# Performance work log

Measured on AMD Instinct MI355X. Metric: run time of the kernel, lower is better.

## Reference

```python
import jax, jax.numpy as jnp
import numpy as np

H = 2304; I_FF = 9216; NH = 8; NKV = 4; HD = 256; W = 4096; V = 65536
EPS = 1e-6; SOFTCAP = 30.0; HALF = HD // 2; POS = W // 2  # current decode position
WSCALE = 0.02


def rmsnorm(x, w, eps=EPS):
    return x * jax.lax.rsqrt(jnp.mean(x * x, axis=-1, keepdims=True) + eps) * w


def setup_inputs() -> dict:
    key = jax.random.key(0)
    ks = jax.random.split(key, 16)
    # RoPE angles for position POS
    inv_freq = 1.0 / (10000.0 ** (jnp.arange(HALF, dtype=jnp.float32) / HALF))
    ang = POS * inv_freq
    # attention mask: allow slots <= POS, block the rest
    slot = jnp.arange(W)
    mask = jnp.where(slot <= POS, 0.0, -1e9).astype(jnp.float32).reshape(1, 1, 1, W)
    # one-hot scatter selector for the cache write
    update_idx = jnp.zeros((1, 1, W, 1), jnp.float32).at[0, 0, POS, 0].set(1.0)
    return {
        "hidden_prev": jax.random.normal(ks[0], (1, 1, H), jnp.float32),
        "embed_token": jax.random.normal(ks[1], (1, 1, H), jnp.float32),
        "kv_k_in": jax.random.normal(ks[2], (1, NKV, W, HD), jnp.float32),
        "kv_v_in": jax.random.normal(ks[3], (1, NKV, W, HD), jnp.float32),
        "cos": jnp.cos(ang),
        "sin": jnp.sin(ang),
        "mask": mask,
        "update_idx": update_idx,
        "in_h_w": jax.random.normal(ks[4], (H, H), jnp.float32) * WSCALE,
        "in_e_w": jax.random.normal(ks[5], (H, H), jnp.float32) * WSCALE,
        "input_ln_w": jnp.ones((H,), jnp.float32),
        "post_attn_ln_w": jnp.ones((H,), jnp.float32),
        "pre_ffn_ln_w": jnp.ones((H,), jnp.float32),
        "post_ffn_ln_w": jnp.ones((H,), jnp.float32),
        "final_ln_w": jnp.ones((H,), jnp.float32),
        "q_w": jax.random.normal(ks[6], (NH * HD, H), jnp.float32) * WSCALE,
        "k_w": jax.random.normal(ks[7], (NKV * HD, H), jnp.float32) * WSCALE,
        "v_w": jax.random.normal(ks[8], (NKV * HD, H), jnp.float32) * WSCALE,
        "o_w": jax.random.normal(ks[9], (H, NH * HD), jnp.float32) * WSCALE,
        "q_norm_w": jnp.ones((HD,), jnp.float32),
        "k_norm_w": jnp.ones((HD,), jnp.float32),
        "gate_w": jax.random.normal(ks[10], (I_FF, H), jnp.float32) * WSCALE,
        "up_w": jax.random.normal(ks[11], (I_FF, H), jnp.float32) * WSCALE,
        "down_w": jax.random.normal(ks[12], (H, I_FF), jnp.float32) * WSCALE,
        "lm_head_w": jax.random.normal(ks[13], (V, H), jnp.float32) * WSCALE,
    }


def reference(hidden_prev, embed_token, kv_k_in, kv_v_in, cos, sin, mask, update_idx,
              in_h_w, in_e_w, input_ln_w, post_attn_ln_w, pre_ffn_ln_w, post_ffn_ln_w,
              final_ln_w, q_w, k_w, v_w, o_w, q_norm_w, k_norm_w, gate_w, up_w, down_w,
              lm_head_w):
    # dual input projection (1x1 convs == linear)
    x = hidden_prev @ in_h_w.T + embed_token @ in_e_w.T          # [1,1,H]
    residual = x
    hn = rmsnorm(x, input_ln_w)
    # QKV
    q = (hn @ q_w.T).reshape(1, NH, 1, HD)
    k = (hn @ k_w.T).reshape(1, NKV, 1, HD)
    v = (hn @ v_w.T).reshape(1, NKV, 1, HD)
    q = rmsnorm(q, q_norm_w)
    k = rmsnorm(k, k_norm_w)
    # RoPE (half-split rotation)
    cos_r = cos.reshape(1, 1, 1, HALF)
    sin_r = sin.reshape(1, 1, 1, HALF)
    q1, q2 = q[..., :HALF], q[..., HALF:]
    q = jnp.concatenate([q1 * cos_r - q2 * sin_r, q2 * cos_r + q1 * sin_r], axis=-1)
    k1, k2 = k[..., :HALF], k[..., HALF:]
    k_rot = jnp.concatenate([k1 * cos_r - k2 * sin_r, k2 * cos_r + k1 * sin_r], axis=-1)
    # multiply-based KV cache update
    keep = 1.0 - update_idx                                      # [1,1,W,1]
    kv_k_out = kv_k_in * keep + k_rot * update_idx               # [1,NKV,W,HD]
    kv_v_out = kv_v_in * keep + v * update_idx
    # GQA expansion
    n_rep = NH // NKV
    k_exp = jnp.repeat(kv_k_out, n_rep, axis=1)                  # [1,NH,W,HD]
    v_exp = jnp.repeat(kv_v_out, n_rep, axis=1)
    # fp32 attention
    scale = 1.0 / np.sqrt(HD)
    attn = jnp.einsum('bhqd,bhkd->bhqk', q, k_exp) * scale + mask
    p = jax.nn.softmax(attn, axis=-1)
    out = jnp.einsum('bhqk,bhkd->bhqd', p, v_exp).reshape(1, 1, NH * HD)
    h_attn = rmsnorm(out @ o_w.T, post_attn_ln_w)
    x = residual + h_attn
    residual = x
    # FFN (gelu-gated)
    hf = rmsnorm(x, pre_ffn_ln_w)
    d = (jax.nn.gelu(hf @ gate_w.T, approximate=False) * (hf @ up_w.T)) @ down_w.T
    x = residual + rmsnorm(d, post_ffn_ln_w)
    hidden_out = rmsnorm(x, final_ln_w)
    # lm_head + softcap + argmax
    logits = hidden_out @ lm_head_w.T                            # [1,1,V]
    logits = jnp.tanh(logits / SOFTCAP) * SOFTCAP
    idx = jnp.argmax(logits, axis=-1)                            # [1,1]
    top_k_indices = idx.reshape(1).astype(jnp.int32)
    top_k_values = jnp.take_along_axis(logits, idx[..., None], axis=-1).reshape(1)
    return (top_k_indices, top_k_values, hidden_out, kv_k_out, kv_v_out)
```

## Files before the change

### kernel.cpp

```cpp
#include <hip/hip_runtime.h>
#include <math.h>

#define H      2304
#define I_FF   9216
#define NH     8
#define NKV    4
#define HD     256
#define W_CTX  4096
#define V_SZ   65536
#define POS    2048
#define NCHUNK 32
#define CHUNK  64
#define NATTN  (NH * NCHUNK)
#define NBLK_ATTN_TOTAL 2048
#define EPS    1e-6f
#define NBLK_IN   576
#define NBLK_LM   4096

enum {
  WS_X    = 0,
  WS_SSQ  = 2304,
  WS_QKV  = 2880,
  WS_ML   = 6976,
  WS_YP   = 7488,
  WS_HRAW = 73024,
  WS_X2   = 75328,
  WS_ACT  = 77632,
  WS_DV   = 86848,
  WS_PART = 89152,
  WS_END  = 97344
};

typedef float f4v __attribute__((ext_vector_type(4)));
typedef float f2v __attribute__((ext_vector_type(2)));

__device__ __forceinline__ f4v ntload4(const float* p) {
  return __builtin_nontemporal_load((const f4v*)p);
}
__device__ __forceinline__ float wave_reduce_sum(float v) {
#pragma unroll
  for (int off = 32; off; off >>= 1) v += __shfl_down(v, off);
  return v;
}
__device__ __forceinline__ float wave_reduce_max(float v) {
#pragma unroll
  for (int off = 32; off; off >>= 1) v = fmaxf(v, __shfl_down(v, off));
  return v;
}
__device__ __forceinline__ float dot4(float4 a, float4 b) {
  return a.x * b.x + a.y * b.y + a.z * b.z + a.w * b.w;
}
__device__ __forceinline__ float dot4n(f4v a, float4 b) {
  return a.x * b.x + a.y * b.y + a.z * b.z + a.w * b.w;
}

__global__ void k_input(const float* __restrict__ Wh, const float* __restrict__ We,
                        const float* __restrict__ hprev, const float* __restrict__ emb,
                        float* __restrict__ x, float* __restrict__ ssq_part) {
  __shared__ float sv[4];
  int wv = threadIdx.x >> 6, lane = threadIdx.x & 63;
  int row = blockIdx.x * 4 + wv;
  const float* wh = Wh + (size_t)row * H;
  const float* we = We + (size_t)row * H;
  const float4* hp = (const float4*)hprev;
  const float4* em = (const float4*)emb;
  float acc = 0.f;
#pragma unroll
  for (int i = 0; i < H / 256; ++i) {
    int idx = lane + i * 64;
    acc += dot4n(ntload4(wh + idx * 4), hp[idx]);
    acc += dot4n(ntload4(we + idx * 4), em[idx]);
  }
  acc = wave_reduce_sum(acc);
  if (lane == 0) { x[row] = acc; sv[wv] = acc * acc; }
  __syncthreads();
  if (threadIdx.x == 0) ssq_part[blockIdx.x] = sv[0] + sv[1] + sv[2] + sv[3];
}

__global__ void k_qkv(const float* __restrict__ qw, const float* __restrict__ kw,
                      const float* __restrict__ vw, const float* __restrict__ x,
                      const float* __restrict__ lnw, const float* __restrict__ ssq,
                      float* __restrict__ qkv) {
  __shared__ float sred[4];
  int tid = threadIdx.x, lane = tid & 63, wv = tid >> 6;
  int row = (blockIdx.x * 256 + tid) >> 6;
  const float* Wrow;
  if (row < 2048)      Wrow = qw + (size_t)row * H;
  else if (row < 3072) Wrow = kw + (size_t)(row - 2048) * H;
  else                 Wrow = vw + (size_t)(row - 3072) * H;
  f4v p0 = ntload4(Wrow + lane * 4);
  float s = ssq[tid] + ssq[tid + 256] + (tid < 64 ? ssq[tid + 512] : 0.f);
  s = wave_reduce_sum(s);
  if (lane == 0) sred[wv] = s;
  __syncthreads();
  float scale = rsqrtf((sred[0] + sred[1] + sred[2] + sred[3]) / (float)H + EPS);

  const float4* xv = (const float4*)x;
  const float4* l4 = (const float4*)lnw;
  float4 hx0 = xv[lane], wl0 = l4[lane];
  float acc = p0.x * (hx0.x * scale * wl0.x) + p0.y * (hx0.y * scale * wl0.y) +
              p0.z * (hx0.z * scale * wl0.z) + p0.w * (hx0.w * scale * wl0.w);
#pragma unroll
  for (int i = 1; i < H / 256; ++i) {
    int idx = lane + i * 64;
    f4v w = ntload4(Wrow + idx * 4);
    float4 hx = xv[idx], wl = l4[idx];
    acc += w.x * (hx.x * scale * wl.x) + w.y * (hx.y * scale * wl.y) +
           w.z * (hx.z * scale * wl.z) + w.w * (hx.w * scale * wl.w);
  }
  acc = wave_reduce_sum(acc);
  if (lane == 0) qkv[row] = acc;
}

__global__ void k_attn(const float* __restrict__ qkv, const float* __restrict__ qnw,
                       const float* __restrict__ knw, const float* __restrict__ cosv,
                       const float* __restrict__ sinv, const float* __restrict__ kin,
                       const float* __restrict__ vin, float* __restrict__ kv_k_out,
                       float* __restrict__ kv_v_out, float* __restrict__ ml,
                       float* __restrict__ ypart,
                       const f2v* __restrict__ kin2, const f2v* __restrict__ vin2,
                       f2v* __restrict__ kout2, f2v* __restrict__ vout2) {
  int b = blockIdx.x;
  int tid = threadIdx.x, lane = tid & 63, wv = tid >> 6;
  if (b >= NATTN) {
    size_t cb = b - NATTN;
    const size_t n = (size_t)NKV * W_CTX * HD / 2;
    const size_t stride = (size_t)(NBLK_ATTN_TOTAL - NATTN) * 256;
    for (size_t i = cb * 256 + tid; i < n; i += stride) {
      int slot = (int)((i >> 7) & (W_CTX - 1));
      if (slot != POS) {
        __builtin_nontemporal_store(kin2[i], kout2 + i);
        __builtin_nontemporal_store(vin2[i], vout2 + i);
      }
    }
    return;
  }
  int h = b >> 5, j = b & 31, kvh = h >> 1;
  __shared__ float qs[HD], ks[HD], sc[CHUNK + 1];
  __shared__ float sredq[4], sredk[4];
  float qv = qkv[h * HD + tid];
  float kv = qkv[2048 + kvh * HD + tid];
  float pq = wave_reduce_sum(qv * qv);
  float pk = wave_reduce_sum(kv * kv);
  if (lane == 0) { sredq[wv] = pq; sredk[wv] = pk; }
  __syncthreads();
  float sq = rsqrtf((sredq[0] + sredq[1] + sredq[2] + sredq[3]) / (float)HD + EPS);
  float sk = rsqrtf((sredk[0] + sredk[1] + sredk[2] + sredk[3]) / (float)HD + EPS);
  qs[tid] = qv * sq * qnw[tid];
  ks[tid] = kv * sk * knw[tid];
  __syncthreads();
  if (tid < HD / 2) {
    float c = cosv[tid], s2 = sinv[tid];
    float q1 = qs[tid], q2 = qs[tid + 128];
    qs[tid] = q1 * c - q2 * s2;  qs[tid + 128] = q2 * c + q1 * s2;
    float k1 = ks[tid], k2 = ks[tid + 128];
    ks[tid] = k1 * c - k2 * s2;  ks[tid + 128] = k2 * c + k1 * s2;
  }
  __syncthreads();
  if (j == 0 && (h & 1) == 0) {
    kv_k_out[((size_t)kvh * W_CTX + POS) * HD + tid] = ks[tid];
    kv_v_out[((size_t)kvh * W_CTX + POS) * HD + tid] = qkv[3072 + kvh * HD + tid];
  }
  int base = j * CHUNK;
  int clen = (j == NCHUNK - 1) ? CHUNK + 1 : CHUNK;
  float4 qf = ((const float4*)qs)[lane];
  const float4* Kb = (const float4*)(kin + ((size_t)kvh * W_CTX + base) * HD);
  for (int i = wv; i < clen; i += 4) {
    float4 kk = (i < CHUNK) ? Kb[(size_t)i * (HD / 4) + lane] : ((const float4*)ks)[lane];
    float acc = dot4(qf, kk);
    acc = wave_reduce_sum(acc);
    if (lane == 0) sc[i] = acc * 0.0625f;
  }
  __syncthreads();
  float m = -1e30f;
  for (int i = tid; i < clen; i += 256) m = fmaxf(m, sc[i]);
  m = wave_reduce_max(m);
  if (lane == 0) sredq[wv] = m;
  __syncthreads();
  float M = fmaxf(fmaxf(sredq[0], sredq[1]), fmaxf(sredq[2], sredq[3]));
  float ssum = 0.f;
  for (int i = tid; i < clen; i += 256) { float e = expf(sc[i] - M); sc[i] = e; ssum += e; }
  ssum = wave_reduce_sum(ssum);
  if (lane == 0) sredk[wv] = ssum;
  __syncthreads();
  if (tid == 0) {
    ml[(h * NCHUNK + j) * 2]     = M;
    ml[(h * NCHUNK + j) * 2 + 1] = sredk[0] + sredk[1] + sredk[2] + sredk[3];
  }
  const float* Vb = vin + ((size_t)kvh * W_CTX + base) * HD;
  float a0 = 0.f, a1 = 0.f, a2 = 0.f, a3 = 0.f;
  for (int s = 0; s < CHUNK; s += 4) {
    a0 += sc[s]     * Vb[(size_t)s * HD + tid];
    a1 += sc[s + 1] * Vb[(size_t)(s + 1) * HD + tid];
    a2 += sc[s + 2] * Vb[(size_t)(s + 2) * HD + tid];
    a3 += sc[s + 3] * Vb[(size_t)(s + 3) * HD + tid];
  }
  if (clen > CHUNK) a0 += sc[CHUNK] * qkv[3072 + kvh * HD + tid];
  ypart[(size_t)(h * NCHUNK + j) * HD + tid] = a0 + a1 + a2 + a3;
}

__global__ void k_o(const float* __restrict__ ow, const float* __restrict__ ml,
                    const float* __restrict__ yp, float* __restrict__ hraw) {
  __shared__ float lmm[256], lml[256], ew[256], Lh[8];
  __shared__ float atts[NH * HD];
  int tid = threadIdx.x, lane = tid & 63, wv = tid >> 6;
  lmm[tid] = ml[2 * tid];
  lml[tid] = ml[2 * tid + 1];
  __syncthreads();
  int hh = tid >> 5;
  float M = -1e30f;
#pragma unroll 8
  for (int jj = 0; jj < 32; ++jj) M = fmaxf(M, lmm[hh * 32 + jj]);
  ew[tid] = expf(lmm[tid] - M);
  __syncthreads();
  if ((tid & 31) == 0) {
    float L = 0.f;
#pragma unroll 8
    for (int jj = 0; jj < 32; ++jj) L += lml[tid + jj] * ew[tid + jj];
    Lh[tid >> 5] = L;
  }
  __syncthreads();
#pragma unroll
  for (int ho = 0; ho < 2; ++ho) {
    int h2 = 2 * wv + ho;
    float4 acc = make_float4(0.f, 0.f, 0.f, 0.f);
#pragma unroll 8
    for (int jj = 0; jj < 32; ++jj) {
      const float4* yr = (const float4*)(yp + (size_t)(h2 * 32 + jj) * HD);
      float4 v = yr[lane];
      float w = ew[h2 * 32 + jj];
      acc.x += w * v.x; acc.y += w * v.y; acc.z += w * v.z; acc.w += w * v.w;
    }
    float invL = 1.f / Lh[h2];
    float4 r = make_float4(acc.x * invL, acc.y * invL, acc.z * invL, acc.w * invL);
    ((float4*)atts)[h2 * (HD / 4) + lane] = r;
  }
  __syncthreads();
  int row = blockIdx.x * 4 + wv;
  const float* wr = ow + (size_t)row * (NH * HD);
  const float4* xv = (const float4*)atts;
  float acc = 0.f;
#pragma unroll
  for (int i = 0; i < (NH * HD) / 256; ++i) {
    int idx = lane + i * 64;
    acc += dot4n(ntload4(wr + idx * 4), xv[idx]);
  }
  acc = wave_reduce_sum(acc);
  if (lane == 0) hraw[row] = acc;
}

__global__ void k_gateup(const float* __restrict__ gw, const float* __restrict__ uw,
                         const float* __restrict__ x, const float* __restrict__ hraw,
                         const float* __restrict__ w_post, const float* __restrict__ w_pre,
                         float* __restrict__ x2_out, float* __restrict__ act) {
  __shared__ float hfs[H];
  __shared__ float srA[4], srB[4];
  int tid = threadIdx.x, lane = tid & 63, wv = tid >> 6;
  int r0 = (blockIdx.x * 4 + wv) * 2;
  const float* g0 = gw + (size_t)r0 * H;
  const float* g1 = gw + (size_t)(r0 + 1) * H;
  const float* u0 = uw + (size_t)r0 * H;
  const float* u1 = uw + (size_t)(r0 + 1) * H;
  f4v pg0 = ntload4(g0 + lane * 4), pg1 = ntload4(g1 + lane * 4);
  f4v pu0 = ntload4(u0 + lane * 4), pu1 = ntload4(u1 + lane * 4);
  float lh[9], lx2[9];
  float ss = 0.f;
#pragma unroll
  for (int k = 0; k < 9; ++k) { lh[k] = hraw[tid + k * 256]; ss += lh[k] * lh[k]; }
  ss = wave_reduce_sum(ss);
  if (lane == 0) srA[wv] = ss;
  __syncthreads();
  float sc1 = rsqrtf((srA[0] + srA[1] + srA[2] + srA[3]) / (float)H + EPS);
  float ss2 = 0.f;
#pragma unroll
  for (int k = 0; k < 9; ++k) {
    int i = tid + k * 256;
    float v = x[i] + lh[k] * sc1 * w_post[i];
    lx2[k] = v; ss2 += v * v;
  }
  ss2 = wave_reduce_sum(ss2);
  if (lane == 0) srB[wv] = ss2;
  __syncthreads();
  float sc2 = rsqrtf((srB[0] + srB[1] + srB[2] + srB[3]) / (float)H + EPS);
#pragma unroll
  for (int k = 0; k < 9; ++k) { int i = tid + k * 256; hfs[i] = lx2[k] * sc2 * w_pre[i]; }
  if (blockIdx.x == 0) {
#pragma unroll
    for (int k = 0; k < 9; ++k) { int i = tid + k * 256; x2_out[i] = lx2[k]; }
  }
  __syncthreads();
  const float4* h4 = (const float4*)hfs;
  float4 hh0 = h4[lane];
  float ag0 = dot4n(pg0, hh0), ag1 = dot4n(pg1, hh0);
  float au0 = dot4n(pu0, hh0), au1 = dot4n(pu1, hh0);
#pragma unroll
  for (int i = 1; i < H / 256; ++i) {
    int idx = lane + i * 64;
    float4 hh = h4[idx];
    ag0 += dot4n(ntload4(g0 + idx * 4), hh);
    ag1 += dot4n(ntload4(g1 + idx * 4), hh);
    au0 += dot4n(ntload4(u0 + idx * 4), hh);
    au1 += dot4n(ntload4(u1 + idx * 4), hh);
  }
  ag0 = wave_reduce_sum(ag0);
  ag1 = wave_reduce_sum(ag1);
  au0 = wave_reduce_sum(au0);
  au1 = wave_reduce_sum(au1);
  if (lane == 0) {
    float gl0 = 0.5f * ag0 * (1.f + erff(ag0 * 0.70710678118f));
    float gl1 = 0.5f * ag1 * (1.f + erff(ag1 * 0.70710678118f));
    act[r0]     = gl0 * au0;
    act[r0 + 1] = gl1 * au1;
  }
}

__global__ void k_down(const float* __restrict__ dw, const float* __restrict__ actv,
                       float* __restrict__ dv) {
  int row  = (blockIdx.x * 256 + threadIdx.x) >> 6;
  int lane = threadIdx.x & 63;
  const float* wr = dw + (size_t)row * I_FF;
  const float4* xv = (const float4*)actv;
  float acc = 0.f;
#pragma unroll 4
  for (int i = 0; i < I_FF / 256; ++i) {
    int idx = lane + i * 64;
    acc += dot4n(ntload4(wr + idx * 4), xv[idx]);
  }
  acc = wave_reduce_sum(acc);
  if (lane == 0) dv[row] = acc;
}

__global__ void k_lmhead(const float* __restrict__ Wm, const float* __restrict__ x2,
                         const float* __restrict__ dv, const float* __restrict__ w_post,
                         const float* __restrict__ w_fin, float* __restrict__ hid_out,
                         float2* __restrict__ partials) {
  __shared__ float hid[H];
  __shared__ float srA[4], srB[4];
  __shared__ float bv[4]; __shared__ int bi[4];
  int tid = threadIdx.x, lane = tid & 63, wv = tid >> 6;
  int gw   = (blockIdx.x * 256 + tid) >> 6;
  int row0 = gw * 4;
  const float* w0 = Wm + (size_t)(row0 + 0) * H;
  const float* w1 = Wm + (size_t)(row0 + 1) * H;
  const float* w2 = Wm + (size_t)(row0 + 2) * H;
  const float* w3 = Wm + (size_t)(row0 + 3) * H;
  f4v p0 = ntload4(w0 + lane * 4), p1 = ntload4(w1 + lane * 4);
  f4v p2 = ntload4(w2 + lane * 4), p3 = ntload4(w3 + lane * 4);
  float ld[9], lx3[9];
  float ss = 0.f;
#pragma unroll
  for (int k = 0; k < 9; ++k) { ld[k] = dv[tid + k * 256]; ss += ld[k] * ld[k]; }
  ss = wave_reduce_sum(ss);
  if (lane == 0) srA[wv] = ss;
  __syncthreads();
  float sc1 = rsqrtf((srA[0] + srA[1] + srA[2] + srA[3]) / (float)H + EPS);
  float ss2 = 0.f;
#pragma unroll
  for (int k = 0; k < 9; ++k) {
    int i = tid + k * 256;
    float v = x2[i] + ld[k] * sc1 * w_post[i];
    lx3[k] = v; ss2 += v * v;
  }
  ss2 = wave_reduce_sum(ss2);
  if (lane == 0) srB[wv] = ss2;
  __syncthreads();
  float sc2 = rsqrtf((srB[0] + srB[1] + srB[2] + srB[3]) / (float)H + EPS);
#pragma unroll
  for (int k = 0; k < 9; ++k) { int i = tid + k * 256; hid[i] = lx3[k] * sc2 * w_fin[i]; }
  if (blockIdx.x == 0) {
#pragma unroll
    for (int k = 0; k < 9; ++k) { int i = tid + k * 256; hid_out[i] = hid[i]; }
  }
  __syncthreads();
  const float4* hv = (const float4*)hid;
  float4 b0 = hv[lane];
  float a0 = dot4n(p0, b0), a1 = dot4n(p1, b0);
  float a2 = dot4n(p2, b0), a3 = dot4n(p3, b0);
#pragma unroll
  for (int i = 1; i < H / 256; ++i) {
    int idx = lane + i * 64;
    float4 b = hv[idx];
    a0 += dot4n(ntload4(w0 + idx * 4), b);
    a1 += dot4n(ntload4(w1 + idx * 4), b);
    a2 += dot4n(ntload4(w2 + idx * 4), b);
    a3 += dot4n(ntload4(w3 + idx * 4), b);
  }
  a0 = wave_reduce_sum(a0);
  a1 = wave_reduce_sum(a1);
  a2 = wave_reduce_sum(a2);
  a3 = wave_reduce_sum(a3);
  if (lane == 0) {
    float l0 = 30.f * tanhf(a0 * (1.f / 30.f));
    float l1 = 30.f * tanhf(a1 * (1.f / 30.f));
    float l2 = 30.f * tanhf(a2 * (1.f / 30.f));
    float l3 = 30.f * tanhf(a3 * (1.f / 30.f));
    float best = l0; int bidx = row0;
    if (l1 > best) { best = l1; bidx = row0 + 1; }
    if (l2 > best) { best = l2; bidx = row0 + 2; }
    if (l3 > best) { best = l3; bidx = row0 + 3; }
    bv[wv] = best; bi[wv] = bidx;
  }
  __syncthreads();
  if (tid == 0) {
    float B = bv[0]; int I = bi[0];
    for (int i = 1; i < 4; ++i)
      if (bv[i] > B || (bv[i] == B && bi[i] < I)) { B = bv[i]; I = bi[i]; }
    partials[blockIdx.x] = make_float2(B, (float)I);
  }
}

__global__ void k_argmax_final(const float2* __restrict__ partials, int n,
                               float* __restrict__ out) {
  __shared__ float bv[256]; __shared__ int bi[256];
  int tid = threadIdx.x;
  float best = -1e30f; int bidx = 0x7fffffff;
  for (int i = tid; i < n; i += 256) {
    float2 p = partials[i];
    int pi = (int)p.y;
    if (p.x > best || (p.x == best && pi < bidx)) { best = p.x; bidx = pi; }
  }
  bv[tid] = best; bi[tid] = bidx; __syncthreads();
  for (int s = 128; s; s >>= 1) {
    if (tid < s) {
      if (bv[tid + s] > bv[tid] || (bv[tid + s] == bv[tid] && bi[tid + s] < bi[tid])) {
        bv[tid] = bv[tid + s]; bi[tid] = bi[tid + s];
      }
    }
    __syncthreads();
  }
  if (tid == 0) { out[0] = (float)bi[0]; out[1] = bv[0]; }
}

extern "C" void kernel_launch(void* const* d_in, const int* in_sizes, int n_in,
                              void* d_out, int out_size, void* d_ws, size_t ws_size,
                              hipStream_t stream) {
  const float* hidden_prev = (const float*)d_in[0];
  const float* embed_token = (const float*)d_in[1];
  const float* kv_k_in     = (const float*)d_in[2];
  const float* kv_v_in     = (const float*)d_in[3];
  const float* cosv        = (const float*)d_in[4];
  const float* sinv        = (const float*)d_in[5];
  const float* in_h_w      = (const float*)d_in[8];
  const float* in_e_w      = (const float*)d_in[9];
  const float* input_ln_w  = (const float*)d_in[10];
  const float* post_attn_w = (const float*)d_in[11];
  const float* pre_ffn_w   = (const float*)d_in[12];
  const float* post_ffn_w  = (const float*)d_in[13];
  const float* final_ln_w  = (const float*)d_in[14];
  const float* q_w         = (const float*)d_in[15];
  const float* k_w         = (const float*)d_in[16];
  const float* v_w         = (const float*)d_in[17];
  const float* o_w         = (const float*)d_in[18];
  const float* q_norm_w    = (const float*)d_in[19];
  const float* k_norm_w    = (const float*)d_in[20];
  const float* gate_w      = (const float*)d_in[21];
  const float* up_w        = (const float*)d_in[22];
  const float* down_w      = (const float*)d_in[23];
  const float* lm_head_w   = (const float*)d_in[24];

  float* out     = (float*)d_out;
  float* out_hid = out + 2;
  float* out_kvk = out + 2 + H;
  float* out_kvv = out_kvk + (size_t)NKV * W_CTX * HD;
  float* ws      = (float*)d_ws;

  k_input<<<NBLK_IN, 256, 0, stream>>>(in_h_w, in_e_w, hidden_prev, embed_token,
                                       ws + WS_X, ws + WS_SSQ);
  k_qkv<<<1024, 256, 0, stream>>>(q_w, k_w, v_w, ws + WS_X, input_ln_w,
                                  ws + WS_SSQ, ws + WS_QKV);
  k_attn<<<NBLK_ATTN_TOTAL, 256, 0, stream>>>(
      ws + WS_QKV, q_norm_w, k_norm_w, cosv, sinv, kv_k_in, kv_v_in,
      out_kvk, out_kvv, ws + WS_ML, ws + WS_YP,
      (const f2v*)kv_k_in, (const f2v*)kv_v_in, (f2v*)out_kvk, (f2v*)out_kvv);
  k_o<<<H / 4, 256, 0, stream>>>(o_w, ws + WS_ML, ws + WS_YP, ws + WS_HRAW);
  k_gateup<<<I_FF / 8, 256, 0, stream>>>(gate_w, up_w, ws + WS_X, ws + WS_HRAW,
                                         post_attn_w, pre_ffn_w, ws + WS_X2, ws + WS_ACT);
  k_down<<<H / 4, 256, 0, stream>>>(down_w, ws + WS_ACT, ws + WS_DV);
  k_lmhead<<<NBLK_LM, 256, 0, stream>>>(lm_head_w, ws + WS_X2, ws + WS_DV,
                                        post_ffn_w, final_ln_w, out_hid,
                                        (float2*)(ws + WS_PART));
  k_argmax_final<<<1, 256, 0, stream>>>((const float2*)(ws + WS_PART), NBLK_LM, out);

  (void)in_sizes; (void)n_in; (void)out_size; (void)ws_size;
}
```

Measured before the change: 196.2 us.

## Widen lm_head rows per wave, fold argmax into atomicMax, halve attention chunks

The lm_head kernel now has each wave compute 8 vocab rows instead of 4, which halves the block count. It drops the separate partials array and argmax kernel by packing an order-preserving float key with the inverted index into a 64-bit atomicMax, and tanh is applied only once to the winning raw logit. Attention uses 16 chunks of 128 slots instead of 32 of 64, and the combine in k_o is adjusted to match. This reduces reduction traffic and per-block overhead, at the cost of more registers per wave and fewer attention blocks, which means less parallelism per head.

```diff
diff --git a/kernel.cpp b/kernel.cpp
--- a/kernel.cpp
+++ b/kernel.cpp
@@ -9,26 +9,26 @@
 #define W_CTX  4096
 #define V_SZ   65536
 #define POS    2048
-#define NCHUNK 32
-#define CHUNK  64
+#define NCHUNK 16
+#define CHUNK  128
 #define NATTN  (NH * NCHUNK)
 #define NBLK_ATTN_TOTAL 2048
 #define EPS    1e-6f
 #define NBLK_IN   576
-#define NBLK_LM   4096
+#define NBLK_LM   2048
 
 enum {
   WS_X    = 0,
   WS_SSQ  = 2304,
-  WS_QKV  = 2880,
-  WS_ML   = 6976,
-  WS_YP   = 7488,
-  WS_HRAW = 73024,
-  WS_X2   = 75328,
-  WS_ACT  = 77632,
-  WS_DV   = 86848,
-  WS_PART = 89152,
-  WS_END  = 97344
+  WS_AMAX = 2880,
+  WS_QKV  = 2896,
+  WS_ML   = 6992,
+  WS_YP   = 7248,
+  WS_HRAW = 40016,
+  WS_X2   = 42320,
+  WS_ACT  = 44624,
+  WS_DV   = 53840,
+  WS_END  = 56144
 };
 
 typedef float f4v __attribute__((ext_vector_type(4)));
@@ -53,10 +53,16 @@
 __device__ __forceinline__ float dot4n(f4v a, float4 b) {
   return a.x * b.x + a.y * b.y + a.z * b.z + a.w * b.w;
 }
+__device__ __forceinline__ unsigned int fkey(float v) {
+  unsigned int b = __float_as_uint(v);
+  return (b & 0x80000000u) ? ~b : (b | 0x80000000u);
+}
 
 __global__ void k_input(const float* __restrict__ Wh, const float* __restrict__ We,
                         const float* __restrict__ hprev, const float* __restrict__ emb,
-                        float* __restrict__ x, float* __restrict__ ssq_part) {
+                        float* __restrict__ x, float* __restrict__ ssq_part,
+                        unsigned long long* __restrict__ amax) {
+  if (blockIdx.x == 0 && threadIdx.x == 0) amax[0] = 0ull;
   __shared__ float sv[4];
   int wv = threadIdx.x >> 6, lane = threadIdx.x & 63;
   int row = blockIdx.x * 4 + wv;
@@ -135,7 +141,7 @@
     }
     return;
   }
-  int h = b >> 5, j = b & 31, kvh = h >> 1;
+  int h = b >> 4, j = b & 15, kvh = h >> 1;
   __shared__ float qs[HD], ks[HD], sc[CHUNK + 1];
   __shared__ float sredq[4], sredk[4];
   float qv = qkv[h * HD + tid];
@@ -201,39 +207,40 @@
 
 __global__ void k_o(const float* __restrict__ ow, const float* __restrict__ ml,
                     const float* __restrict__ yp, float* __restrict__ hraw) {
-  __shared__ float lmm[256], lml[256], ew[256], Lh[8];
+  __shared__ float lmm[128], lml[128], ew[128], Lh[8];
   __shared__ float atts[NH * HD];
   int tid = threadIdx.x, lane = tid & 63, wv = tid >> 6;
-  lmm[tid] = ml[2 * tid];
-  lml[tid] = ml[2 * tid + 1];
-  __syncthreads();
-  int hh = tid >> 5;
-  float M = -1e30f;
-#pragma unroll 8
-  for (int jj = 0; jj < 32; ++jj) M = fmaxf(M, lmm[hh * 32 + jj]);
-  ew[tid] = expf(lmm[tid] - M);
-  __syncthreads();
-  if ((tid & 31) == 0) {
+  if (tid < 128) { lmm[tid] = ml[2 * tid]; lml[tid] = ml[2 * tid + 1]; }
+  __syncthreads();
+  if (tid < 128) {
+    int hh = tid >> 4;
+    float M = -1e30f;
+#pragma unroll
+    for (int jj = 0; jj < NCHUNK; ++jj) M = fmaxf(M, lmm[hh * NCHUNK + jj]);
+    ew[tid] = expf(lmm[tid] - M);
+  }
+  __syncthreads();
+  if (tid < 128 && (tid & 15) == 0) {
     float L = 0.f;
-#pragma unroll 8
-    for (int jj = 0; jj < 32; ++jj) L += lml[tid + jj] * ew[tid + jj];
-    Lh[tid >> 5] = L;
+#pragma unroll
+    for (int jj = 0; jj < NCHUNK; ++jj) L += lml[tid + jj] * ew[tid + jj];
+    Lh[tid >> 4] = L;
   }
   __syncthreads();
 #pragma unroll
   for (int ho = 0; ho < 2; ++ho) {
     int h2 = 2 * wv + ho;
     float4 acc = make_float4(0.f, 0.f, 0.f, 0.f);
-#pragma unroll 8
-    for (int jj = 0; jj < 32; ++jj) {
-      const float4* yr = (const float4*)(yp + (size_t)(h2 * 32 + jj) * HD);
+#pragma unroll
+    for (int jj = 0; jj < NCHUNK; ++jj) {
+      const float4* yr = (const float4*)(yp + (size_t)(h2 * NCHUNK + jj) * HD);
       float4 v = yr[lane];
-      float w = ew[h2 * 32 + jj];
+      float w = ew[h2 * NCHUNK + jj];
       acc.x += w * v.x; acc.y += w * v.y; acc.z += w * v.z; acc.w += w * v.w;
     }
     float invL = 1.f / Lh[h2];
-    float4 r = make_float4(acc.x * invL, acc.y * invL, acc.z * invL, acc.w * invL);
-    ((float4*)atts)[h2 * (HD / 4) + lane] = r;
+    ((float4*)atts)[h2 * (HD / 4) + lane] =
+        make_float4(acc.x * invL, acc.y * invL, acc.z * invL, acc.w * invL);
   }
   __syncthreads();
   int row = blockIdx.x * 4 + wv;
@@ -333,17 +340,20 @@
 __global__ void k_lmhead(const float* __restrict__ Wm, const float* __restrict__ x2,
                          const float* __restrict__ dv, const float* __restrict__ w_post,
                          const float* __restrict__ w_fin, float* __restrict__ hid_out,
-                         float2* __restrict__ partials) {
+                         unsigned long long* __restrict__ amax) {
   __shared__ float hid[H];
   __shared__ float srA[4], srB[4];
-  __shared__ float bv[4]; __shared__ int bi[4];
+  __shared__ unsigned long long wbest[4];
   int tid = threadIdx.x, lane = tid & 63, wv = tid >> 6;
-  int gw   = (blockIdx.x * 256 + tid) >> 6;
-  int row0 = gw * 4;
+  int row0 = (blockIdx.x * 4 + wv) * 8;
   const float* w0 = Wm + (size_t)(row0 + 0) * H;
   const float* w1 = Wm + (size_t)(row0 + 1) * H;
   const float* w2 = Wm + (size_t)(row0 + 2) * H;
   const float* w3 = Wm + (size_t)(row0 + 3) * H;
+  const float* w4 = Wm + (size_t)(row0 + 4) * H;
+  const float* w5 = Wm + (size_t)(row0 + 5) * H;
+  const float* w6 = Wm + (size_t)(row0 + 6) * H;
+  const float* w7 = Wm + (size_t)(row0 + 7) * H;
   f4v p0 = ntload4(w0 + lane * 4), p1 = ntload4(w1 + lane * 4);
   f4v p2 = ntload4(w2 + lane * 4), p3 = ntload4(w3 + lane * 4);
   float ld[9], lx3[9];
@@ -376,6 +386,10 @@
   float4 b0 = hv[lane];
   float a0 = dot4n(p0, b0), a1 = dot4n(p1, b0);
   float a2 = dot4n(p2, b0), a3 = dot4n(p3, b0);
+  float a4 = dot4n(ntload4(w4 + lane * 4), b0);
+  float a5 = dot4n(ntload4(w5 + lane * 4), b0);
+  float a6 = dot4n(ntload4(w6 + lane * 4), b0);
+  float a7 = dot4n(ntload4(w7 + lane * 4), b0);
 #pragma unroll
   for (int i = 1; i < H / 256; ++i) {
     int idx = lane + i * 64;
@@ -384,51 +398,48 @@
     a1 += dot4n(ntload4(w1 + idx * 4), b);
     a2 += dot4n(ntload4(w2 + idx * 4), b);
     a3 += dot4n(ntload4(w3 + idx * 4), b);
+    a4 += dot4n(ntload4(w4 + idx * 4), b);
+    a5 += dot4n(ntload4(w5 + idx * 4), b);
+    a6 += dot4n(ntload4(w6 + idx * 4), b);
+    a7 += dot4n(ntload4(w7 + idx * 4), b);
   }
   a0 = wave_reduce_sum(a0);
   a1 = wave_reduce_sum(a1);
   a2 = wave_reduce_sum(a2);
   a3 = wave_reduce_sum(a3);
+  a4 = wave_reduce_sum(a4);
+  a5 = wave_reduce_sum(a5);
+  a6 = wave_reduce_sum(a6);
+  a7 = wave_reduce_sum(a7);
   if (lane == 0) {
-    float l0 = 30.f * tanhf(a0 * (1.f / 30.f));
-    float l1 = 30.f * tanhf(a1 * (1.f / 30.f));
-    float l2 = 30.f * tanhf(a2 * (1.f / 30.f));
-    float l3 = 30.f * tanhf(a3 * (1.f / 30.f));
-    float best = l0; int bidx = row0;
-    if (l1 > best) { best = l1; bidx = row0 + 1; }
-    if (l2 > best) { best = l2; bidx = row0 + 2; }
-    if (l3 > best) { best = l3; bidx = row0 + 3; }
-    bv[wv] = best; bi[wv] = bidx;
+    float va[8] = {a0, a1, a2, a3, a4, a5, a6, a7};
+    float best = va[0]; int bidx = row0;
+#pragma unroll
+    for (int r = 1; r < 8; ++r)
+      if (va[r] > best) { best = va[r]; bidx = row0 + r; }
+    wbest[wv] = ((unsigned long long)fkey(best) << 32) |
+                (0xFFFFFFFFu - (unsigned int)bidx);
   }
   __syncthreads();
   if (tid == 0) {
-    float B = bv[0]; int I = bi[0];
-    for (int i = 1; i < 4; ++i)
-      if (bv[i] > B || (bv[i] == B && bi[i] < I)) { B = bv[i]; I = bi[i]; }
-    partials[blockIdx.x] = make_float2(B, (float)I);
-  }
-}
-
-__global__ void k_argmax_final(const float2* __restrict__ partials, int n,
-                               float* __restrict__ out) {
-  __shared__ float bv[256]; __shared__ int bi[256];
-  int tid = threadIdx.x;
-  float best = -1e30f; int bidx = 0x7fffffff;
-  for (int i = tid; i < n; i += 256) {
-    float2 p = partials[i];
-    int pi = (int)p.y;
-    if (p.x > best || (p.x == best && pi < bidx)) { best = p.x; bidx = pi; }
-  }
-  bv[tid] = best; bi[tid] = bidx; __syncthreads();
-  for (int s = 128; s; s >>= 1) {
-    if (tid < s) {
-      if (bv[tid + s] > bv[tid] || (bv[tid + s] == bv[tid] && bi[tid + s] < bi[tid])) {
-        bv[tid] = bv[tid + s]; bi[tid] = bi[tid + s];
-      }
-    }
-    __syncthreads();
-  }
-  if (tid == 0) { out[0] = (float)bi[0]; out[1] = bv[0]; }
+    unsigned long long B = wbest[0];
+    for (int i = 1; i < 4; ++i) B = (wbest[i] > B) ? wbest[i] : B;
+    atomicMax(amax, B);
+  }
+}
+
+__global__ void k_decode(const unsigned long long* __restrict__ amax,
+                         float* __restrict__ out) {
+  if (threadIdx.x == 0) {
+    unsigned long long k = amax[0];
+    unsigned int key32  = (unsigned int)(k >> 32);
+    unsigned int idxkey = (unsigned int)k;
+    unsigned int bits = (key32 & 0x80000000u) ? (key32 ^ 0x80000000u) : ~key32;
+    float raw = __uint_as_float(bits);
+    int row = (int)(0xFFFFFFFFu - idxkey);
+    out[0] = (float)row;
+    out[1] = 30.f * tanhf(raw * (1.f / 30.f));
+  }
 }
 
 extern "C" void kernel_launch(void* const* d_in, const int* in_sizes, int n_in,
@@ -463,9 +474,10 @@
   float* out_kvk = out + 2 + H;
   float* out_kvv = out_kvk + (size_t)NKV * W_CTX * HD;
   float* ws      = (float*)d_ws;
+  unsigned long long* amax = (unsigned long long*)(ws + WS_AMAX);
 
   k_input<<<NBLK_IN, 256, 0, stream>>>(in_h_w, in_e_w, hidden_prev, embed_token,
-                                       ws + WS_X, ws + WS_SSQ);
+                                       ws + WS_X, ws + WS_SSQ, amax);
   k_qkv<<<1024, 256, 0, stream>>>(q_w, k_w, v_w, ws + WS_X, input_ln_w,
                                   ws + WS_SSQ, ws + WS_QKV);
   k_attn<<<NBLK_ATTN_TOTAL, 256, 0, stream>>>(
@@ -477,9 +489,8 @@
                                          post_attn_w, pre_ffn_w, ws + WS_X2, ws + WS_ACT);
   k_down<<<H / 4, 256, 0, stream>>>(down_w, ws + WS_ACT, ws + WS_DV);
   k_lmhead<<<NBLK_LM, 256, 0, stream>>>(lm_head_w, ws + WS_X2, ws + WS_DV,
-                                        post_ffn_w, final_ln_w, out_hid,
-                                        (float2*)(ws + WS_PART));
-  k_argmax_final<<<1, 256, 0, stream>>>((const float2*)(ws + WS_PART), NBLK_LM, out);
+                                        post_ffn_w, final_ln_w, out_hid, amax);
+  k_decode<<<1, 64, 0, stream>>>(amax, out);
 
   (void)in_sizes; (void)n_in; (void)out_size; (void)ws_size;
 }
```

Result: slower. 218.6 us (+11.4%).
